# Optimization experiments

Measured on AMD Instinct MI355X. Metric: run time of the kernel, lower is better.

## Reference

```python
import jax, jax.numpy as jnp
import numpy as np

K = 3  # spatial window (window_size = [1,3,3,1])


def _extract_patches(x, k):
    """TF-style extract_patches, VALID padding, stride 1, rate 1.
    x: [B,H,W,C] -> [B,Ho,Wo,k*k*C] with depth ordering (ki, kj, c)."""
    B, H, W, C = x.shape
    Ho, Wo = H - k + 1, W - k + 1
    cols = [x[:, ki:ki + Ho, kj:kj + Wo, :] for ki in range(k) for kj in range(k)]
    return jnp.concatenate(cols, axis=-1)


def setup_inputs() -> dict:
    key = jax.random.key(0)
    k1, k2 = jax.random.split(key)
    x = jax.random.normal(k1, (8, 32, 32, 32), dtype=jnp.float32)
    # weight shape per build(): (1, 1, 1, K*K*C, filters) = (1,1,1,288,64)
    w = jax.random.normal(k2, (1, 1, 1, 3 * 3 * 32, 64), dtype=jnp.float32) * 0.05
    bias = jnp.zeros((64,), dtype=jnp.float32)
    return {"x": x, "w": w, "bias": bias}


def reference(x, w, bias):
    # patches: [B,Ho,Wo,KKC]
    p = _extract_patches(x, K)
    # broadcast add: [B,Ho,Wo,KKC,1] + [KKC,F] -> [B,Ho,Wo,KKC,F]
    r = p[..., None] + w[0, 0, 0]
    # tropical conv: max-plus minus min-plus over the patch axis, plus bias
    return jnp.max(r, axis=3) - jnp.min(r, axis=3) + bias
```

## Files before the change

kernel.cpp:

```cpp
#include <hip/hip_runtime.h>
#include <math.h>


#define COLP 36

__global__ __launch_bounds__(256) void trop_kernel(
    const float* __restrict__ x, const float* __restrict__ w,
    const float* __restrict__ bias, float* __restrict__ out) {
  __shared__ float wl[96 * 64];
  __shared__ float xt[3 * 32 * COLP];

  const int b = blockIdx.x / 30;
  const int i = blockIdx.x % 30;
  const int tid = threadIdx.x;
  const int f = tid & 63;
  const int wave = tid >> 6;
  const int j0 = wave * 8;

  float mx[8], mn[8];
#pragma unroll
  for (int p = 0; p < 8; ++p) { mx[p] = -INFINITY; mn[p] = INFINITY; }

  const float* xb = x + (((size_t)b * 32 + i) * 32) * 32;
#pragma unroll
  for (int t = 0; t < 3; ++t) {
    int idx = tid + t * 256;
    int ki = idx >> 8;
    int rem = idx & 255;
    int col = rem >> 3;
    int c4 = (rem & 7) * 4;
    float4 v = *(const float4*)(xb + ((size_t)(ki * 32 + col)) * 32 + c4);
    float* dst = &xt[(ki * 32 + c4) * COLP + col];
    dst[0 * COLP] = v.x;
    dst[1 * COLP] = v.y;
    dst[2 * COLP] = v.z;
    dst[3 * COLP] = v.w;
  }

  for (int ki = 0; ki < 3; ++ki) {
    __syncthreads();
    const float4* wg = (const float4*)(w + ki * 96 * 64);
    float4* wld = (float4*)wl;
#pragma unroll
    for (int t = 0; t < 6; ++t) {
      wld[tid + t * 256] = wg[tid + t * 256];
    }
    __syncthreads();

#pragma unroll
    for (int c = 0; c < 32; ++c) {
      const float* row = &xt[(ki * 32 + c) * COLP];
      float4 a = *(const float4*)(row + j0);
      float4 bq = *(const float4*)(row + j0 + 4);
      float4 cq = *(const float4*)(row + j0 + 8);
      float xr[12] = {a.x, a.y, a.z, a.w, bq.x, bq.y, bq.z, bq.w,
                      cq.x, cq.y, cq.z, cq.w};
#pragma unroll
      for (int kj = 0; kj < 3; ++kj) {
        float wval = wl[(kj * 32 + c) * 64 + f];
#pragma unroll
        for (int p = 0; p < 8; ++p) {
          float t2 = xr[p + kj] + wval;
          mx[p] = fmaxf(mx[p], t2);
          mn[p] = fminf(mn[p], t2);
        }
      }
    }
  }

  float bv = bias[f];
  float* ob = out + (((size_t)b * 30 + i) * 30) * 64 + f;
#pragma unroll
  for (int p = 0; p < 8; ++p) {
    int j = j0 + p;
    if (j < 30) ob[(size_t)j * 64] = mx[p] - mn[p] + bv;
  }
}

extern "C" void kernel_launch(void* const* d_in, const int* in_sizes, int n_in,
                              void* d_out, int out_size, void* d_ws, size_t ws_size,
                              hipStream_t stream) {
  const float* x = (const float*)d_in[0];
  const float* w = (const float*)d_in[1];
  const float* bias = (const float*)d_in[2];
  float* out = (float*)d_out;
  dim3 grid(8 * 30);
  dim3 block(256);
  hipLaunchKernelGGL(trop_kernel, grid, block, 0, stream, x, w, bias, out);
}
```

Baseline: 75.43 us.

## Split output columns across blocks to raise grid parallelism

The grid changes from 240 blocks, each covering a full output row, to 960 blocks that each cover 8 output columns. Each thread now computes 2 outputs instead of 8, and the staged input tile shrinks to 10 columns. The aim is to fill more of the GPU's compute units and cut per-thread serial work. In exchange, every block reloads the full weight tensor into shared memory, so weight traffic rises fourfold and per-output reuse of loaded weights drops.

```diff
diff --git a/kernel.cpp b/kernel.cpp
--- a/kernel.cpp
+++ b/kernel.cpp
@@ -2,79 +2,72 @@
 #include <math.h>
 
 
-#define COLP 36
+#define NCOL 10
 
 __global__ __launch_bounds__(256) void trop_kernel(
     const float* __restrict__ x, const float* __restrict__ w,
     const float* __restrict__ bias, float* __restrict__ out) {
   __shared__ float wl[96 * 64];
-  __shared__ float xt[3 * 32 * COLP];
+  __shared__ float xt[3 * 32 * NCOL];
 
-  const int b = blockIdx.x / 30;
-  const int i = blockIdx.x % 30;
+  const int jg = blockIdx.x;
+  const int i = blockIdx.y;
+  const int b = blockIdx.z;
   const int tid = threadIdx.x;
   const int f = tid & 63;
   const int wave = tid >> 6;
-  const int j0 = wave * 8;
-
-  float mx[8], mn[8];
-#pragma unroll
-  for (int p = 0; p < 8; ++p) { mx[p] = -INFINITY; mn[p] = INFINITY; }
+  const int jw = wave * 2;
+  const int j0 = jg * 8;
 
   const float* xb = x + (((size_t)b * 32 + i) * 32) * 32;
-#pragma unroll
-  for (int t = 0; t < 3; ++t) {
-    int idx = tid + t * 256;
-    int ki = idx >> 8;
-    int rem = idx & 255;
-    int col = rem >> 3;
-    int c4 = (rem & 7) * 4;
-    float4 v = *(const float4*)(xb + ((size_t)(ki * 32 + col)) * 32 + c4);
-    float* dst = &xt[(ki * 32 + c4) * COLP + col];
-    dst[0 * COLP] = v.x;
-    dst[1 * COLP] = v.y;
-    dst[2 * COLP] = v.z;
-    dst[3 * COLP] = v.w;
+  if (tid < 240) {
+    int ki = tid / 80;
+    int rem = tid % 80;
+    int col = rem / 8;
+    int c4 = (rem % 8) * 4;
+    if (j0 + col < 32) {
+      float4 v = *(const float4*)(xb + ((size_t)(ki * 32 + j0 + col)) * 32 + c4);
+      xt[(ki * 32 + c4 + 0) * NCOL + col] = v.x;
+      xt[(ki * 32 + c4 + 1) * NCOL + col] = v.y;
+      xt[(ki * 32 + c4 + 2) * NCOL + col] = v.z;
+      xt[(ki * 32 + c4 + 3) * NCOL + col] = v.w;
+    }
   }
+
+  float mx0 = -INFINITY, mx1 = -INFINITY;
+  float mn0 = INFINITY, mn1 = INFINITY;
 
   for (int ki = 0; ki < 3; ++ki) {
     __syncthreads();
     const float4* wg = (const float4*)(w + ki * 96 * 64);
     float4* wld = (float4*)wl;
 #pragma unroll
-    for (int t = 0; t < 6; ++t) {
-      wld[tid + t * 256] = wg[tid + t * 256];
-    }
+    for (int t = 0; t < 6; ++t) wld[tid + t * 256] = wg[tid + t * 256];
     __syncthreads();
 
 #pragma unroll
     for (int c = 0; c < 32; ++c) {
-      const float* row = &xt[(ki * 32 + c) * COLP];
-      float4 a = *(const float4*)(row + j0);
-      float4 bq = *(const float4*)(row + j0 + 4);
-      float4 cq = *(const float4*)(row + j0 + 8);
-      float xr[12] = {a.x, a.y, a.z, a.w, bq.x, bq.y, bq.z, bq.w,
-                      cq.x, cq.y, cq.z, cq.w};
-#pragma unroll
-      for (int kj = 0; kj < 3; ++kj) {
-        float wval = wl[(kj * 32 + c) * 64 + f];
-#pragma unroll
-        for (int p = 0; p < 8; ++p) {
-          float t2 = xr[p + kj] + wval;
-          mx[p] = fmaxf(mx[p], t2);
-          mn[p] = fminf(mn[p], t2);
-        }
-      }
+      const float* row = &xt[(ki * 32 + c) * NCOL];
+      float2 a = *(const float2*)(row + jw);
+      float2 d = *(const float2*)(row + jw + 2);
+      float w0 = wl[(0 * 32 + c) * 64 + f];
+      float w1 = wl[(1 * 32 + c) * 64 + f];
+      float w2 = wl[(2 * 32 + c) * 64 + f];
+      float t00 = a.x + w0, t01 = a.y + w0;
+      float t10 = a.y + w1, t11 = d.x + w1;
+      float t20 = d.x + w2, t21 = d.y + w2;
+      mx0 = fmaxf(mx0, fmaxf(t00, fmaxf(t10, t20)));
+      mx1 = fmaxf(mx1, fmaxf(t01, fmaxf(t11, t21)));
+      mn0 = fminf(mn0, fminf(t00, fminf(t10, t20)));
+      mn1 = fminf(mn1, fminf(t01, fminf(t11, t21)));
     }
   }
 
   float bv = bias[f];
   float* ob = out + (((size_t)b * 30 + i) * 30) * 64 + f;
-#pragma unroll
-  for (int p = 0; p < 8; ++p) {
-    int j = j0 + p;
-    if (j < 30) ob[(size_t)j * 64] = mx[p] - mn[p] + bv;
-  }
+  int j = j0 + jw;
+  if (j < 30) ob[(size_t)j * 64] = mx0 - mn0 + bv;
+  if (j + 1 < 30) ob[(size_t)(j + 1) * 64] = mx1 - mn1 + bv;
 }
 
 extern "C" void kernel_launch(void* const* d_in, const int* in_sizes, int n_in,
@@ -84,7 +77,7 @@
   const float* w = (const float*)d_in[1];
   const float* bias = (const float*)d_in[2];
   float* out = (float*)d_out;
-  dim3 grid(8 * 30);
+  dim3 grid(4, 30, 8);
   dim3 block(256);
   hipLaunchKernelGGL(trop_kernel, grid, block, 0, stream, x, w, bias, out);
 }
```

Measured after the change: 71.78 us. 4.8% less time.
